# Kernel optimization log

Measured on AMD Instinct MI355X. Metric: run time of the kernel, lower is better.

Reference implementation:

```python
import jax, jax.numpy as jnp
import numpy as np

D_MODEL = 1024
NUM_HEADS = 16
MAX_SEQ_LEN = 2048
THETA = 10000.0
D_K = D_MODEL // NUM_HEADS


def setup_inputs() -> dict:
    key = jax.random.key(0)
    ks = jax.random.split(key, 5)
    B, S = 4, MAX_SEQ_LEN
    std = 2.0 / (D_MODEL + D_MODEL)
    x = jax.random.normal(ks[0], (B, S, D_MODEL), dtype=jnp.float32)
    Wq = jax.random.normal(ks[1], (D_MODEL, D_MODEL), dtype=jnp.float32) * std
    Wk = jax.random.normal(ks[2], (D_MODEL, D_MODEL), dtype=jnp.float32) * std
    Wv = jax.random.normal(ks[3], (D_MODEL, D_MODEL), dtype=jnp.float32) * std
    Wo = jax.random.normal(ks[4], (D_MODEL, D_MODEL), dtype=jnp.float32) * std
    token_positions = jnp.arange(S, dtype=jnp.int64) if jax.config.jax_enable_x64 else jnp.arange(S, dtype=jnp.int32)
    return {"x": x, "token_positions": token_positions, "Wq": Wq, "Wk": Wk, "Wv": Wv, "Wo": Wo}


def _rope_tables(token_positions):
    # angles[i, j] = pos_i / theta^(2j/d_k),  j in [0, d_k/2)
    k = jnp.arange(0, D_K, 2, dtype=jnp.float32)
    inv_freq = 1.0 / (THETA ** (k / D_K))  # [d_k/2]
    angles = token_positions.astype(jnp.float32)[:, None] * inv_freq[None, :]  # [s, d_k/2]
    return jnp.sin(angles), jnp.cos(angles)


def _apply_rope(x, sin, cos):
    # x: [b, h, s, d_k], sin/cos: [s, d_k/2] broadcast over b,h
    x_even = x[..., 0::2]
    x_odd = x[..., 1::2]
    out_even = x_even * cos - x_odd * sin
    out_odd = x_odd * cos + x_even * sin
    # interleave back: [..., d_k/2, 2] -> [..., d_k]
    return jnp.stack([out_even, out_odd], axis=-1).reshape(x.shape)


def reference(x, token_positions, Wq, Wk, Wv, Wo):
    B, S, _ = x.shape
    H, Dk = NUM_HEADS, D_K

    def proj(W):
        y = jnp.einsum('oi,bsi->bso', W, x)
        return y.reshape(B, S, H, Dk).transpose(0, 2, 1, 3)  # [b, h, s, d_k]

    q, k, v = proj(Wq), proj(Wk), proj(Wv)
    sin, cos = _rope_tables(token_positions)
    q = _apply_rope(q, sin, cos)
    k = _apply_rope(k, sin, cos)

    scores = jnp.einsum('bhqd,bhkd->bhqk', q, k) / jnp.sqrt(jnp.float32(Dk))
    mask = jnp.tril(jnp.ones((S, S), dtype=bool))  # causal
    scores = jnp.where(mask[None, None], scores, -jnp.inf)
    attn = jax.nn.softmax(scores, axis=-1)
    out = jnp.einsum('bhqk,bhkd->bhqd', attn, v)
    out = out.transpose(0, 2, 1, 3).reshape(B, S, H * Dk)
    return jnp.einsum('oi,bsi->bso', Wo, out)
```

## Files before the change

kernel.cpp:

```cpp
#include <hip/hip_runtime.h>
#include <math.h>

#define S_LEN 2048
#define NHEADS 16
#define DK 64

typedef _Float16 h4 __attribute__((ext_vector_type(4)));
typedef _Float16 h8 __attribute__((ext_vector_type(8)));
typedef float f4 __attribute__((ext_vector_type(4)));

__device__ __forceinline__ void glds16(const void* g, void* l) {
  __builtin_amdgcn_global_load_lds(
      (const __attribute__((address_space(1))) unsigned int*)g,
      (__attribute__((address_space(3))) unsigned int*)l, 16, 0, 0);
}

__global__ void rope_table_kernel(const int* __restrict__ pos,
                                  float* __restrict__ sin_t,
                                  float* __restrict__ cos_t) {
  int idx = blockIdx.x * blockDim.x + threadIdx.x;
  if (idx >= S_LEN * 32) return;
  int s = idx >> 5, p = idx & 31;
  double inv = pow(10000.0, -(double)(2 * p) / 64.0);
  double a = (double)pos[s] * inv;
  sin_t[idx] = (float)sin(a);
  cos_t[idx] = (float)cos(a);
}

__global__ __launch_bounds__(256) void cvt_x_kernel(const float* __restrict__ src,
                                                    _Float16* __restrict__ dst) {
  int i = blockIdx.x * 256 + threadIdx.x;
  float4 v = *(const float4*)(src + (size_t)i * 4);
  h4 o = {(_Float16)v.x, (_Float16)v.y, (_Float16)v.z, (_Float16)v.w};
  *(h4*)&dst[(size_t)i * 4] = o;
}

__global__ __launch_bounds__(256) void cvt_w_kernel(
    const float* __restrict__ w0, const float* __restrict__ w1,
    const float* __restrict__ w2, const float* __restrict__ w3,
    _Float16* __restrict__ dst) {
  int i = blockIdx.x * 256 + threadIdx.x;
  const float* srcs[4] = {w0, w1, w2, w3};
  int which = i >> 18;
  int off = (i & 262143) * 4;
  float4 v = *(const float4*)(srcs[which] + off);
  h4 o = {(_Float16)(v.x * 256.f), (_Float16)(v.y * 256.f),
          (_Float16)(v.z * 256.f), (_Float16)(v.w * 256.f)};
  *(h4*)&dst[(size_t)which * 1048576 + off] = o;
}

__global__ __launch_bounds__(256) void gemm_f16_nt(
    const _Float16* __restrict__ A, const _Float16* __restrict__ B,
    float* __restrict__ C32, _Float16* __restrict__ C16,
    const float* __restrict__ sin_t, const float* __restrict__ cos_t,
    int mode) {
  __shared__ _Float16 As[128 * 32];
  __shared__ _Float16 Bs[128 * 32];
  const int t = threadIdx.x;
  const int lane = t & 63;
  const int w = t >> 6;
  const int m0 = blockIdx.y * 128;
  const int n0 = blockIdx.x * 128;
  const int wm = (w >> 1) * 64;
  const int wn = (w & 1) * 64;
  const int lm = lane & 15;
  const int kq = (lane >> 4) * 8;
  const int srow = lane >> 2;
  const int skof = (lane & 3) * 8;

  f4 acc[4][4];
#pragma unroll
  for (int i = 0; i < 4; i++)
#pragma unroll
    for (int j = 0; j < 4; j++) {
      f4 z = {0.f, 0.f, 0.f, 0.f};
      acc[i][j] = z;
    }

  for (int k0 = 0; k0 < 1024; k0 += 32) {
    __syncthreads();
#pragma unroll
    for (int c = 0; c < 2; c++) {
      int rr = (w + c * 4) * 16 + srow;
      glds16(A + (size_t)(m0 + rr) * 1024 + k0 + skof, (char*)As + (w + c * 4) * 1024);
      glds16(B + (size_t)(n0 + rr) * 1024 + k0 + skof, (char*)Bs + (w + c * 4) * 1024);
    }
    __syncthreads();

    h8 af[4], bf[4];
#pragma unroll
    for (int mt = 0; mt < 4; mt++)
      af[mt] = *(const h8*)(As + (wm + mt * 16 + lm) * 32 + kq);
#pragma unroll
    for (int nt = 0; nt < 4; nt++)
      bf[nt] = *(const h8*)(Bs + (wn + nt * 16 + lm) * 32 + kq);
#pragma unroll
    for (int mt = 0; mt < 4; mt++)
#pragma unroll
      for (int nt = 0; nt < 4; nt++)
        acc[mt][nt] = __builtin_amdgcn_mfma_f32_16x16x32_f16(af[mt], bf[nt],
                                                             acc[mt][nt], 0, 0, 0);
  }

  const float scale = 1.0f / 256.0f;
  const int qrow = lane >> 4;
#pragma unroll
  for (int mt = 0; mt < 4; mt++) {
#pragma unroll
    for (int nt = 0; nt < 4; nt++) {
      int n = n0 + wn + nt * 16 + lm;
      if (mode == 1) {
        int d = n & 63, h = n >> 6;
        int mbase = m0 + wm + mt * 16 + qrow * 4;
        int s = mbase & (S_LEN - 1), b = mbase >> 11;
        h4 ov = {(_Float16)(acc[mt][nt][0] * scale), (_Float16)(acc[mt][nt][1] * scale),
                 (_Float16)(acc[mt][nt][2] * scale), (_Float16)(acc[mt][nt][3] * scale)};
        *(h4*)&C16[(((size_t)b * NHEADS + h) * DK + d) * S_LEN + s] = ov;
      } else {
#pragma unroll
        for (int r = 0; r < 4; r++) {
          int m = m0 + wm + mt * 16 + qrow * 4 + r;
          float v = acc[mt][nt][r] * scale;
          if (mode == 0) {
            C32[(size_t)m * 1024 + n] = v;
          } else {
            int s = m & (S_LEN - 1), b = m >> 11;
            int d = n & 63, h = n >> 6;
            float partner = __shfl_xor(v, 1);
            int p = d >> 1;
            float sn = sin_t[s * 32 + p], cs = cos_t[s * 32 + p];
            v = (d & 1) ? (v * cs + partner * sn) : (v * cs - partner * sn);
            C16[(((size_t)b * NHEADS + h) * S_LEN + s) * DK + d] = (_Float16)v;
          }
        }
      }
    }
  }
}

__global__ __launch_bounds__(256) void attn_mfma(
    const _Float16* __restrict__ Q, const _Float16* __restrict__ K,
    const _Float16* __restrict__ Vt, _Float16* __restrict__ O) {
  __shared__ _Float16 Ks[64 * 72];
  __shared__ _Float16 Vs[64 * 72];
  __shared__ _Float16 Ps[128 * 72];

  const int bh = blockIdx.x;
  const int qt = (gridDim.y - 1) - blockIdx.y;
  const int q0 = qt * 128;
  const int t = threadIdx.x;
  const int lane = t & 63;
  const int w = t >> 6;
  const int lm = lane & 15;
  const int quad = lane >> 4;
  const size_t qkbase = (size_t)bh * S_LEN * DK;
  const size_t vbase  = (size_t)bh * DK * S_LEN;

  const int srow = t >> 2;
  const int scol = (t & 3) * 16;

  h8 qf[2][2];
#pragma unroll
  for (int nt = 0; nt < 2; nt++)
#pragma unroll
    for (int kc = 0; kc < 2; kc++) {
      h8 v = *(const h8*)(Q + qkbase + (size_t)(q0 + w * 32 + nt * 16 + lm) * DK +
                          kc * 32 + quad * 8);
#pragma unroll
      for (int j = 0; j < 8; j++) v[j] = v[j] * (_Float16)0.125f;
      qf[nt][kc] = v;
    }

  f4 oacc[4][2];
#pragma unroll
  for (int mt = 0; mt < 4; mt++)
#pragma unroll
    for (int nt = 0; nt < 2; nt++) {
      f4 z = {0.f, 0.f, 0.f, 0.f};
      oacc[mt][nt] = z;
    }
  float m_i[2] = {-INFINITY, -INFINITY};
  float l_i[2] = {0.f, 0.f};

  const int ktmax = (q0 >> 6) + 1;
  for (int kt = 0; kt <= ktmax; kt++) {
    __syncthreads();
    {
      const _Float16* kg = K + qkbase + (size_t)(kt * 64 + srow) * DK + scol;
      const _Float16* vg = Vt + vbase + (size_t)srow * S_LEN + kt * 64 + scol;
      h8 k0 = *(const h8*)kg;
      h8 k1 = *(const h8*)(kg + 8);
      h8 v0 = *(const h8*)vg;
      h8 v1 = *(const h8*)(vg + 8);
      *(h8*)&Ks[srow * 72 + scol] = k0;
      *(h8*)&Ks[srow * 72 + scol + 8] = k1;
      *(h8*)&Vs[srow * 72 + scol] = v0;
      *(h8*)&Vs[srow * 72 + scol + 8] = v1;
    }
    __syncthreads();

    f4 s_[4][2];
#pragma unroll
    for (int mt = 0; mt < 4; mt++)
#pragma unroll
      for (int nt = 0; nt < 2; nt++) {
        f4 z = {0.f, 0.f, 0.f, 0.f};
        s_[mt][nt] = z;
      }
#pragma unroll
    for (int kc = 0; kc < 2; kc++) {
      h8 kf[4];
#pragma unroll
      for (int mt = 0; mt < 4; mt++)
        kf[mt] = *(const h8*)&Ks[(mt * 16 + lm) * 72 + kc * 32 + quad * 8];
#pragma unroll
      for (int mt = 0; mt < 4; mt++)
#pragma unroll
        for (int nt = 0; nt < 2; nt++)
          s_[mt][nt] = __builtin_amdgcn_mfma_f32_16x16x32_f16(kf[mt], qf[nt][kc],
                                                              s_[mt][nt], 0, 0, 0);
    }

    if (kt * 64 + 63 > q0 + w * 32) {
#pragma unroll
      for (int nt = 0; nt < 2; nt++) {
        int srq = q0 + w * 32 + nt * 16 + lm;
#pragma unroll
        for (int mt = 0; mt < 4; mt++)
#pragma unroll
          for (int r = 0; r < 4; r++)
            if (kt * 64 + mt * 16 + quad * 4 + r > srq) s_[mt][nt][r] = -INFINITY;
      }
    }

#pragma unroll
    for (int nt = 0; nt < 2; nt++) {
      float mx = -INFINITY;
#pragma unroll
      for (int mt = 0; mt < 4; mt++)
#pragma unroll
        for (int r = 0; r < 4; r++) mx = fmaxf(mx, s_[mt][nt][r]);
      mx = fmaxf(mx, __shfl_xor(mx, 16));
      mx = fmaxf(mx, __shfl_xor(mx, 32));
      float mnew = fmaxf(m_i[nt], mx);
      float alpha = __expf(m_i[nt] - mnew);
      float sum = 0.f;
#pragma unroll
      for (int mt = 0; mt < 4; mt++) {
#pragma unroll
        for (int r = 0; r < 4; r++) {
          float p = __expf(s_[mt][nt][r] - mnew);
          s_[mt][nt][r] = p;
          sum += p;
        }
      }
      sum += __shfl_xor(sum, 16);
      sum += __shfl_xor(sum, 32);
      m_i[nt] = mnew;
      l_i[nt] = l_i[nt] * alpha + sum;
#pragma unroll
      for (int mt = 0; mt < 4; mt++) {
        oacc[mt][nt][0] *= alpha; oacc[mt][nt][1] *= alpha;
        oacc[mt][nt][2] *= alpha; oacc[mt][nt][3] *= alpha;
        h4 pv = {(_Float16)s_[mt][nt][0], (_Float16)s_[mt][nt][1],
                 (_Float16)s_[mt][nt][2], (_Float16)s_[mt][nt][3]};
        *(h4*)&Ps[(w * 32 + nt * 16 + lm) * 72 + mt * 16 + quad * 4] = pv;
      }
    }
    __syncthreads();

#pragma unroll
    for (int kc = 0; kc < 2; kc++) {
      h8 vf[4], pf[2];
#pragma unroll
      for (int mt = 0; mt < 4; mt++)
        vf[mt] = *(const h8*)&Vs[(mt * 16 + lm) * 72 + kc * 32 + quad * 8];
#pragma unroll
      for (int nt = 0; nt < 2; nt++)
        pf[nt] = *(const h8*)&Ps[(w * 32 + nt * 16 + lm) * 72 + kc * 32 + quad * 8];
#pragma unroll
      for (int mt = 0; mt < 4; mt++)
#pragma unroll
        for (int nt = 0; nt < 2; nt++)
          oacc[mt][nt] = __builtin_amdgcn_mfma_f32_16x16x32_f16(vf[mt], pf[nt],
                                                                oacc[mt][nt], 0, 0, 0);
    }
  }

  const int b = bh >> 4, head = bh & 15;
#pragma unroll
  for (int nt = 0; nt < 2; nt++) {
    float inv = 1.0f / l_i[nt];
    int s = q0 + w * 32 + nt * 16 + lm;
#pragma unroll
    for (int mt = 0; mt < 4; mt++) {
      h4 ov = {(_Float16)(oacc[mt][nt][0] * inv), (_Float16)(oacc[mt][nt][1] * inv),
               (_Float16)(oacc[mt][nt][2] * inv), (_Float16)(oacc[mt][nt][3] * inv)};
      *(h4*)&O[((size_t)b * S_LEN + s) * 1024 + head * 64 + mt * 16 + quad * 4] = ov;
    }
  }
}

extern "C" void kernel_launch(void* const* d_in, const int* in_sizes, int n_in,
                              void* d_out, int out_size, void* d_ws, size_t ws_size,
                              hipStream_t stream) {
  const float* x   = (const float*)d_in[0];
  const int*   pos = (const int*)d_in[1];
  const float* Wq  = (const float*)d_in[2];
  const float* Wk  = (const float*)d_in[3];
  const float* Wv  = (const float*)d_in[4];
  const float* Wo  = (const float*)d_in[5];
  float* out = (float*)d_out;
  (void)in_sizes; (void)n_in; (void)out_size; (void)ws_size;

  const size_t NT = (size_t)4 * S_LEN * 1024;
  _Float16* q16 = (_Float16*)d_ws;
  _Float16* k16 = q16 + NT;
  _Float16* vt16 = k16 + NT;
  _Float16* aoh = vt16 + NT;
  _Float16* xh  = aoh + NT;
  _Float16* wh  = xh + NT;
  float* sin_t = (float*)(wh + 4 * 1048576);
  float* cos_t = sin_t + S_LEN * 32;

  rope_table_kernel<<<(S_LEN * 32 + 255) / 256, 256, 0, stream>>>(pos, sin_t, cos_t);
  cvt_x_kernel<<<8192, 256, 0, stream>>>(x, xh);
  cvt_w_kernel<<<4096, 256, 0, stream>>>(Wq, Wk, Wv, Wo, wh);

  dim3 gg(8, 64);
  gemm_f16_nt<<<gg, 256, 0, stream>>>(xh, wh,           nullptr, q16, sin_t, cos_t, 2);
  gemm_f16_nt<<<gg, 256, 0, stream>>>(xh, wh + 1048576, nullptr, k16, sin_t, cos_t, 2);
  gemm_f16_nt<<<gg, 256, 0, stream>>>(xh, wh + 2097152, nullptr, vt16, nullptr, nullptr, 1);

  dim3 ag(64, S_LEN / 128);
  attn_mfma<<<ag, 256, 0, stream>>>(q16, k16, vt16, aoh);

  gemm_f16_nt<<<gg, 256, 0, stream>>>(aoh, wh + 3145728, out, nullptr, nullptr, nullptr, 0);
}
```

Baseline: 319.3 us.

## Fuse QKV GEMMs and conversions, prefetch K/V tiles and skip masked attention tiles

Merges the x and weight conversion kernels into one launch and the three Q/K/V projection GEMMs into a single 24x64 grid launch. The rope sin/cos tables are interleaved so each lookup is one float2 load. The attention kernel register-prefetches the next K/V tile while the current one is consumed, skips score and PV work for warps whose rows are fully masked, and only rescales the accumulators when the running max grows. The intent is to cut launch overhead, expose more parallelism in the projections, and hide global load latency in attention, at the cost of extra registers in the attention loop.

```diff
diff --git a/kernel.cpp b/kernel.cpp
--- a/kernel.cpp
+++ b/kernel.cpp
@@ -16,51 +16,52 @@
 }
 
 __global__ void rope_table_kernel(const int* __restrict__ pos,
-                                  float* __restrict__ sin_t,
-                                  float* __restrict__ cos_t) {
+                                  float* __restrict__ sc) {
   int idx = blockIdx.x * blockDim.x + threadIdx.x;
   if (idx >= S_LEN * 32) return;
   int s = idx >> 5, p = idx & 31;
   double inv = pow(10000.0, -(double)(2 * p) / 64.0);
   double a = (double)pos[s] * inv;
-  sin_t[idx] = (float)sin(a);
-  cos_t[idx] = (float)cos(a);
-}
-
-__global__ __launch_bounds__(256) void cvt_x_kernel(const float* __restrict__ src,
-                                                    _Float16* __restrict__ dst) {
-  int i = blockIdx.x * 256 + threadIdx.x;
-  float4 v = *(const float4*)(src + (size_t)i * 4);
-  h4 o = {(_Float16)v.x, (_Float16)v.y, (_Float16)v.z, (_Float16)v.w};
-  *(h4*)&dst[(size_t)i * 4] = o;
-}
-
-__global__ __launch_bounds__(256) void cvt_w_kernel(
+  sc[s * 64 + 2 * p]     = (float)sin(a);
+  sc[s * 64 + 2 * p + 1] = (float)cos(a);
+}
+
+__global__ __launch_bounds__(256) void cvt_all(
+    const float* __restrict__ x,
     const float* __restrict__ w0, const float* __restrict__ w1,
     const float* __restrict__ w2, const float* __restrict__ w3,
-    _Float16* __restrict__ dst) {
-  int i = blockIdx.x * 256 + threadIdx.x;
-  const float* srcs[4] = {w0, w1, w2, w3};
-  int which = i >> 18;
-  int off = (i & 262143) * 4;
-  float4 v = *(const float4*)(srcs[which] + off);
-  h4 o = {(_Float16)(v.x * 256.f), (_Float16)(v.y * 256.f),
-          (_Float16)(v.z * 256.f), (_Float16)(v.w * 256.f)};
-  *(h4*)&dst[(size_t)which * 1048576 + off] = o;
-}
-
-__global__ __launch_bounds__(256) void gemm_f16_nt(
-    const _Float16* __restrict__ A, const _Float16* __restrict__ B,
-    float* __restrict__ C32, _Float16* __restrict__ C16,
-    const float* __restrict__ sin_t, const float* __restrict__ cos_t,
-    int mode) {
+    _Float16* __restrict__ xh, _Float16* __restrict__ wh) {
+  int bid = blockIdx.x;
+  if (bid < 8192) {
+    int i = bid * 256 + threadIdx.x;
+    float4 v = *(const float4*)(x + (size_t)i * 4);
+    h4 o = {(_Float16)v.x, (_Float16)v.y, (_Float16)v.z, (_Float16)v.w};
+    *(h4*)&xh[(size_t)i * 4] = o;
+  } else {
+    int j = (bid - 8192) * 256 + threadIdx.x;
+    const float* srcs[4] = {w0, w1, w2, w3};
+    int which = j >> 18;
+    int off = (j & 262143) * 4;
+    float4 v = *(const float4*)(srcs[which] + off);
+    h4 o = {(_Float16)(v.x * 256.f), (_Float16)(v.y * 256.f),
+            (_Float16)(v.z * 256.f), (_Float16)(v.w * 256.f)};
+    *(h4*)&wh[(size_t)which * 1048576 + off] = o;
+  }
+}
+
+__global__ __launch_bounds__(256) void gemm_qkv(
+    const _Float16* __restrict__ A, const _Float16* __restrict__ W3,
+    _Float16* __restrict__ Qo, _Float16* __restrict__ Ko,
+    _Float16* __restrict__ Vto, const float* __restrict__ sc_t) {
   __shared__ _Float16 As[128 * 32];
   __shared__ _Float16 Bs[128 * 32];
   const int t = threadIdx.x;
   const int lane = t & 63;
   const int w = t >> 6;
+  const int mat = blockIdx.x >> 3;
+  const int n0 = (blockIdx.x & 7) * 128;
   const int m0 = blockIdx.y * 128;
-  const int n0 = blockIdx.x * 128;
+  const _Float16* B = W3 + (size_t)mat * 1048576;
   const int wm = (w >> 1) * 64;
   const int wn = (w & 1) * 64;
   const int lm = lane & 15;
@@ -103,39 +104,100 @@
   }
 
   const float scale = 1.0f / 256.0f;
-  const int qrow = lane >> 4;
+  const int quad = lane >> 4;
 #pragma unroll
   for (int mt = 0; mt < 4; mt++) {
 #pragma unroll
     for (int nt = 0; nt < 4; nt++) {
       int n = n0 + wn + nt * 16 + lm;
-      if (mode == 1) {
-        int d = n & 63, h = n >> 6;
-        int mbase = m0 + wm + mt * 16 + qrow * 4;
-        int s = mbase & (S_LEN - 1), b = mbase >> 11;
+      int d = n & 63, h = n >> 6;
+      int mbase = m0 + wm + mt * 16 + quad * 4;
+      int s = mbase & (S_LEN - 1), b = mbase >> 11;
+      if (mat == 2) {
         h4 ov = {(_Float16)(acc[mt][nt][0] * scale), (_Float16)(acc[mt][nt][1] * scale),
                  (_Float16)(acc[mt][nt][2] * scale), (_Float16)(acc[mt][nt][3] * scale)};
-        *(h4*)&C16[(((size_t)b * NHEADS + h) * DK + d) * S_LEN + s] = ov;
+        *(h4*)&Vto[(((size_t)b * NHEADS + h) * DK + d) * S_LEN + s] = ov;
       } else {
+        _Float16* C16 = (mat == 0) ? Qo : Ko;
+        int p2 = d & ~1;
 #pragma unroll
         for (int r = 0; r < 4; r++) {
-          int m = m0 + wm + mt * 16 + qrow * 4 + r;
           float v = acc[mt][nt][r] * scale;
-          if (mode == 0) {
-            C32[(size_t)m * 1024 + n] = v;
-          } else {
-            int s = m & (S_LEN - 1), b = m >> 11;
-            int d = n & 63, h = n >> 6;
-            float partner = __shfl_xor(v, 1);
-            int p = d >> 1;
-            float sn = sin_t[s * 32 + p], cs = cos_t[s * 32 + p];
-            v = (d & 1) ? (v * cs + partner * sn) : (v * cs - partner * sn);
-            C16[(((size_t)b * NHEADS + h) * S_LEN + s) * DK + d] = (_Float16)v;
-          }
+          float2 sc = *(const float2*)&sc_t[(s + r) * 64 + p2];
+          float partner = __shfl_xor(v, 1);
+          v = (d & 1) ? fmaf(v, sc.y, partner * sc.x)
+                      : fmaf(v, sc.y, -partner * sc.x);
+          C16[(((size_t)b * NHEADS + h) * S_LEN + (s + r)) * DK + d] = (_Float16)v;
         }
       }
     }
   }
+}
+
+__global__ __launch_bounds__(256) void gemm_out(
+    const _Float16* __restrict__ A, const _Float16* __restrict__ B,
+    float* __restrict__ C32) {
+  __shared__ _Float16 As[128 * 32];
+  __shared__ _Float16 Bs[128 * 32];
+  const int t = threadIdx.x;
+  const int lane = t & 63;
+  const int w = t >> 6;
+  const int n0 = blockIdx.x * 128;
+  const int m0 = blockIdx.y * 128;
+  const int wm = (w >> 1) * 64;
+  const int wn = (w & 1) * 64;
+  const int lm = lane & 15;
+  const int kq = (lane >> 4) * 8;
+  const int srow = lane >> 2;
+  const int skof = (lane & 3) * 8;
+
+  f4 acc[4][4];
+#pragma unroll
+  for (int i = 0; i < 4; i++)
+#pragma unroll
+    for (int j = 0; j < 4; j++) {
+      f4 z = {0.f, 0.f, 0.f, 0.f};
+      acc[i][j] = z;
+    }
+
+  for (int k0 = 0; k0 < 1024; k0 += 32) {
+    __syncthreads();
+#pragma unroll
+    for (int c = 0; c < 2; c++) {
+      int rr = (w + c * 4) * 16 + srow;
+      glds16(A + (size_t)(m0 + rr) * 1024 + k0 + skof, (char*)As + (w + c * 4) * 1024);
+      glds16(B + (size_t)(n0 + rr) * 1024 + k0 + skof, (char*)Bs + (w + c * 4) * 1024);
+    }
+    __syncthreads();
+
+    h8 af[4], bf[4];
+#pragma unroll
+    for (int mt = 0; mt < 4; mt++)
+      af[mt] = *(const h8*)(As + (wm + mt * 16 + lm) * 32 + kq);
+#pragma unroll
+    for (int nt = 0; nt < 4; nt++)
+      bf[nt] = *(const h8*)(Bs + (wn + nt * 16 + lm) * 32 + kq);
+#pragma unroll
+    for (int mt = 0; mt < 4; mt++)
+#pragma unroll
+      for (int nt = 0; nt < 4; nt++)
+        acc[mt][nt] = __builtin_amdgcn_mfma_f32_16x16x32_f16(af[mt], bf[nt],
+                                                             acc[mt][nt], 0, 0, 0);
+  }
+
+  const float scale = 1.0f / 256.0f;
+  const int quad = lane >> 4;
+#pragma unroll
+  for (int mt = 0; mt < 4; mt++)
+#pragma unroll
+    for (int nt = 0; nt < 4; nt++) {
+      int n = n0 + wn + nt * 16 + lm;
+#pragma unroll
+      for (int r = 0; r < 4; r++) {
+        int m = m0 + wm + mt * 16 + quad * 4 + r;
+        C32[(size_t)m * 1024 + n] = acc[mt][nt][r] * scale;
+      }
+    }
 }
 
 __global__ __launch_bounds__(256) void attn_mfma(
@@ -155,16 +217,16 @@
   const int quad = lane >> 4;
   const size_t qkbase = (size_t)bh * S_LEN * DK;
   const size_t vbase  = (size_t)bh * DK * S_LEN;
-
   const int srow = t >> 2;
   const int scol = (t & 3) * 16;
+  const int wq0 = q0 + w * 32;
 
   h8 qf[2][2];
 #pragma unroll
   for (int nt = 0; nt < 2; nt++)
 #pragma unroll
     for (int kc = 0; kc < 2; kc++) {
-      h8 v = *(const h8*)(Q + qkbase + (size_t)(q0 + w * 32 + nt * 16 + lm) * DK +
+      h8 v = *(const h8*)(Q + qkbase + (size_t)(wq0 + nt * 16 + lm) * DK +
                           kc * 32 + quad * 8);
 #pragma unroll
       for (int j = 0; j < 8; j++) v[j] = v[j] * (_Float16)0.125f;
@@ -182,108 +244,119 @@
   float m_i[2] = {-INFINITY, -INFINITY};
   float l_i[2] = {0.f, 0.f};
 
-  const int ktmax = (q0 >> 6) + 1;
+  const int ktmax = 2 * qt + 1;
+  const _Float16* kg = K + qkbase + (size_t)srow * DK + scol;
+  const _Float16* vg = Vt + vbase + (size_t)srow * S_LEN + scol;
+  h8 pk0 = *(const h8*)kg;
+  h8 pk1 = *(const h8*)(kg + 8);
+  h8 pv0 = *(const h8*)vg;
+  h8 pv1 = *(const h8*)(vg + 8);
+
   for (int kt = 0; kt <= ktmax; kt++) {
     __syncthreads();
-    {
-      const _Float16* kg = K + qkbase + (size_t)(kt * 64 + srow) * DK + scol;
-      const _Float16* vg = Vt + vbase + (size_t)srow * S_LEN + kt * 64 + scol;
-      h8 k0 = *(const h8*)kg;
-      h8 k1 = *(const h8*)(kg + 8);
-      h8 v0 = *(const h8*)vg;
-      h8 v1 = *(const h8*)(vg + 8);
-      *(h8*)&Ks[srow * 72 + scol] = k0;
-      *(h8*)&Ks[srow * 72 + scol + 8] = k1;
-      *(h8*)&Vs[srow * 72 + scol] = v0;
-      *(h8*)&Vs[srow * 72 + scol + 8] = v1;
-    }
-    __syncthreads();
-
-    f4 s_[4][2];
-#pragma unroll
-    for (int mt = 0; mt < 4; mt++)
+    *(h8*)&Ks[srow * 72 + scol] = pk0;
+    *(h8*)&Ks[srow * 72 + scol + 8] = pk1;
+    *(h8*)&Vs[srow * 72 + scol] = pv0;
+    *(h8*)&Vs[srow * 72 + scol + 8] = pv1;
+    if (kt < ktmax) {
+      const _Float16* kgn = kg + (size_t)(kt + 1) * 64 * DK;
+      const _Float16* vgn = vg + (kt + 1) * 64;
+      pk0 = *(const h8*)kgn;
+      pk1 = *(const h8*)(kgn + 8);
+      pv0 = *(const h8*)vgn;
+      pv1 = *(const h8*)(vgn + 8);
+    }
+    __syncthreads();
+
+    if (kt * 64 <= wq0 + 31) {
+      f4 s_[4][2];
+#pragma unroll
+      for (int mt = 0; mt < 4; mt++)
+#pragma unroll
+        for (int nt = 0; nt < 2; nt++) {
+          f4 z = {0.f, 0.f, 0.f, 0.f};
+          s_[mt][nt] = z;
+        }
+#pragma unroll
+      for (int kc = 0; kc < 2; kc++) {
+        h8 kf[4];
+#pragma unroll
+        for (int mt = 0; mt < 4; mt++)
+          kf[mt] = *(const h8*)&Ks[(mt * 16 + lm) * 72 + kc * 32 + quad * 8];
+#pragma unroll
+        for (int mt = 0; mt < 4; mt++)
+#pragma unroll
+          for (int nt = 0; nt < 2; nt++)
+            s_[mt][nt] = __builtin_amdgcn_mfma_f32_16x16x32_f16(kf[mt], qf[nt][kc],
+                                                                s_[mt][nt], 0, 0, 0);
+      }
+
+      if (kt * 64 + 63 > wq0) {
+#pragma unroll
+        for (int nt = 0; nt < 2; nt++) {
+          int srq = wq0 + nt * 16 + lm;
+#pragma unroll
+          for (int mt = 0; mt < 4; mt++)
+#pragma unroll
+            for (int r = 0; r < 4; r++)
+              if (kt * 64 + mt * 16 + quad * 4 + r > srq) s_[mt][nt][r] = -INFINITY;
+        }
+      }
+
 #pragma unroll
       for (int nt = 0; nt < 2; nt++) {
-        f4 z = {0.f, 0.f, 0.f, 0.f};
-        s_[mt][nt] = z;
-      }
-#pragma unroll
-    for (int kc = 0; kc < 2; kc++) {
-      h8 kf[4];
-#pragma unroll
-      for (int mt = 0; mt < 4; mt++)
-        kf[mt] = *(const h8*)&Ks[(mt * 16 + lm) * 72 + kc * 32 + quad * 8];
-#pragma unroll
-      for (int mt = 0; mt < 4; mt++)
+        float mx = -INFINITY;
+#pragma unroll
+        for (int mt = 0; mt < 4; mt++)
+#pragma unroll
+          for (int r = 0; r < 4; r++) mx = fmaxf(mx, s_[mt][nt][r]);
+        mx = fmaxf(mx, __shfl_xor(mx, 16));
+        mx = fmaxf(mx, __shfl_xor(mx, 32));
+        const bool grow = __any(mx > m_i[nt]);
+        const float mnew = grow ? fmaxf(m_i[nt], mx) : m_i[nt];
+        float sum = 0.f;
+#pragma unroll
+        for (int mt = 0; mt < 4; mt++) {
+          float p0 = __expf(s_[mt][nt][0] - mnew);
+          float p1 = __expf(s_[mt][nt][1] - mnew);
+          float p2 = __expf(s_[mt][nt][2] - mnew);
+          float p3 = __expf(s_[mt][nt][3] - mnew);
+          sum += (p0 + p1) + (p2 + p3);
+          h4 pv = {(_Float16)p0, (_Float16)p1, (_Float16)p2, (_Float16)p3};
+          *(h4*)&Ps[(w * 32 + nt * 16 + lm) * 72 + mt * 16 + quad * 4] = pv;
+        }
+        sum += __shfl_xor(sum, 16);
+        sum += __shfl_xor(sum, 32);
+        if (grow) {
+          float alpha = __expf(m_i[nt] - mnew);
+          m_i[nt] = mnew;
+          l_i[nt] = fmaf(l_i[nt], alpha, sum);
+#pragma unroll
+          for (int mt = 0; mt < 4; mt++) {
+            oacc[mt][nt][0] *= alpha; oacc[mt][nt][1] *= alpha;
+            oacc[mt][nt][2] *= alpha; oacc[mt][nt][3] *= alpha;
+          }
+        } else {
+          l_i[nt] += sum;
+        }
+      }
+
+#pragma unroll
+      for (int kc = 0; kc < 2; kc++) {
+        h8 vf[4], pf[2];
+#pragma unroll
+        for (int mt = 0; mt < 4; mt++)
+          vf[mt] = *(const h8*)&Vs[(mt * 16 + lm) * 72 + kc * 32 + quad * 8];
 #pragma unroll
         for (int nt = 0; nt < 2; nt++)
-          s_[mt][nt] = __builtin_amdgcn_mfma_f32_16x16x32_f16(kf[mt], qf[nt][kc],
-                                                              s_[mt][nt], 0, 0, 0);
-    }
-
-    if (kt * 64 + 63 > q0 + w * 32) {
-#pragma unroll
-      for (int nt = 0; nt < 2; nt++) {
-        int srq = q0 + w * 32 + nt * 16 + lm;
+          pf[nt] = *(const h8*)&Ps[(w * 32 + nt * 16 + lm) * 72 + kc * 32 + quad * 8];
 #pragma unroll
         for (int mt = 0; mt < 4; mt++)
 #pragma unroll
-          for (int r = 0; r < 4; r++)
-            if (kt * 64 + mt * 16 + quad * 4 + r > srq) s_[mt][nt][r] = -INFINITY;
-      }
-    }
-
-#pragma unroll
-    for (int nt = 0; nt < 2; nt++) {
-      float mx = -INFINITY;
-#pragma unroll
-      for (int mt = 0; mt < 4; mt++)
-#pragma unroll
-        for (int r = 0; r < 4; r++) mx = fmaxf(mx, s_[mt][nt][r]);
-      mx = fmaxf(mx, __shfl_xor(mx, 16));
-      mx = fmaxf(mx, __shfl_xor(mx, 32));
-      float mnew = fmaxf(m_i[nt], mx);
-      float alpha = __expf(m_i[nt] - mnew);
-      float sum = 0.f;
-#pragma unroll
-      for (int mt = 0; mt < 4; mt++) {
-#pragma unroll
-        for (int r = 0; r < 4; r++) {
-          float p = __expf(s_[mt][nt][r] - mnew);
-          s_[mt][nt][r] = p;
-          sum += p;
-        }
-      }
-      sum += __shfl_xor(sum, 16);
-      sum += __shfl_xor(sum, 32);
-      m_i[nt] = mnew;
-      l_i[nt] = l_i[nt] * alpha + sum;
-#pragma unroll
-      for (int mt = 0; mt < 4; mt++) {
-        oacc[mt][nt][0] *= alpha; oacc[mt][nt][1] *= alpha;
-        oacc[mt][nt][2] *= alpha; oacc[mt][nt][3] *= alpha;
-        h4 pv = {(_Float16)s_[mt][nt][0], (_Float16)s_[mt][nt][1],
-                 (_Float16)s_[mt][nt][2], (_Float16)s_[mt][nt][3]};
-        *(h4*)&Ps[(w * 32 + nt * 16 + lm) * 72 + mt * 16 + quad * 4] = pv;
-      }
-    }
-    __syncthreads();
-
-#pragma unroll
-    for (int kc = 0; kc < 2; kc++) {
-      h8 vf[4], pf[2];
-#pragma unroll
-      for (int mt = 0; mt < 4; mt++)
-        vf[mt] = *(const h8*)&Vs[(mt * 16 + lm) * 72 + kc * 32 + quad * 8];
-#pragma unroll
-      for (int nt = 0; nt < 2; nt++)
-        pf[nt] = *(const h8*)&Ps[(w * 32 + nt * 16 + lm) * 72 + kc * 32 + quad * 8];
-#pragma unroll
-      for (int mt = 0; mt < 4; mt++)
-#pragma unroll
-        for (int nt = 0; nt < 2; nt++)
-          oacc[mt][nt] = __builtin_amdgcn_mfma_f32_16x16x32_f16(vf[mt], pf[nt],
-                                                                oacc[mt][nt], 0, 0, 0);
+          for (int nt = 0; nt < 2; nt++)
+            oacc[mt][nt] = __builtin_amdgcn_mfma_f32_16x16x32_f16(vf[mt], pf[nt],
+                                                                  oacc[mt][nt], 0, 0, 0);
+      }
     }
   }
 
@@ -291,7 +364,7 @@
 #pragma unroll
   for (int nt = 0; nt < 2; nt++) {
     float inv = 1.0f / l_i[nt];
-    int s = q0 + w * 32 + nt * 16 + lm;
+    int s = wq0 + nt * 16 + lm;
 #pragma unroll
     for (int mt = 0; mt < 4; mt++) {
       h4 ov = {(_Float16)(oacc[mt][nt][0] * inv), (_Float16)(oacc[mt][nt][1] * inv),
@@ -314,26 +387,20 @@
   (void)in_sizes; (void)n_in; (void)out_size; (void)ws_size;
 
   const size_t NT = (size_t)4 * S_LEN * 1024;
-  _Float16* q16 = (_Float16*)d_ws;
-  _Float16* k16 = q16 + NT;
+  _Float16* q16  = (_Float16*)d_ws;
+  _Float16* k16  = q16 + NT;
   _Float16* vt16 = k16 + NT;
-  _Float16* aoh = vt16 + NT;
-  _Float16* xh  = aoh + NT;
-  _Float16* wh  = xh + NT;
-  float* sin_t = (float*)(wh + 4 * 1048576);
-  float* cos_t = sin_t + S_LEN * 32;
-
-  rope_table_kernel<<<(S_LEN * 32 + 255) / 256, 256, 0, stream>>>(pos, sin_t, cos_t);
-  cvt_x_kernel<<<8192, 256, 0, stream>>>(x, xh);
-  cvt_w_kernel<<<4096, 256, 0, stream>>>(Wq, Wk, Wv, Wo, wh);
-
-  dim3 gg(8, 64);
-  gemm_f16_nt<<<gg, 256, 0, stream>>>(xh, wh,           nullptr, q16, sin_t, cos_t, 2);
-  gemm_f16_nt<<<gg, 256, 0, stream>>>(xh, wh + 1048576, nullptr, k16, sin_t, cos_t, 2);
-  gemm_f16_nt<<<gg, 256, 0, stream>>>(xh, wh + 2097152, nullptr, vt16, nullptr, nullptr, 1);
-
-  dim3 ag(64, S_LEN / 128);
-  attn_mfma<<<ag, 256, 0, stream>>>(q16, k16, vt16, aoh);
-
-  gemm_f16_nt<<<gg, 256, 0, stream>>>(aoh, wh + 3145728, out, nullptr, nullptr, nullptr, 0);
-}
+  _Float16* aoh  = vt16 + NT;
+  _Float16* xh   = aoh + NT;
+  _Float16* wh   = xh + NT;
+  float* sc_t = (float*)(wh + 4 * 1048576);
+
+  rope_table_kernel<<<256, 256, 0, stream>>>(pos, sc_t);
+  cvt_all<<<12288, 256, 0, stream>>>(x, Wq, Wk, Wv, Wo, xh, wh);
+
+  gemm_qkv<<<dim3(24, 64), 256, 0, stream>>>(xh, wh, q16, k16, vt16, sc_t);
+
+  attn_mfma<<<dim3(64, S_LEN / 128), 256, 0, stream>>>(q16, k16, vt16, aoh);
+
+  gemm_out<<<dim3(8, 64), 256, 0, stream>>>(aoh, wh + 3145728, out);
+}
```

After: 277.4 us. 1.15x faster.
